# Kernel optimization log

Hardware: AMD Instinct MI355X
Metric: run time of the kernel (lower is better)

The kernel has to match this reference:

```python
import jax, jax.numpy as jnp
import numpy as np

D = 768
H = 12
HD = 64
S = 77
FF = 3072
EPS = 1e-5


def _layernorm(x, w, b):
    mu = jnp.mean(x, axis=-1, keepdims=True)
    var = jnp.mean(jnp.square(x - mu), axis=-1, keepdims=True)
    return (x - mu) * jax.lax.rsqrt(var + EPS) * w + b


def setup_inputs() -> dict:
    key = jax.random.key(0)
    ks = jax.random.split(key, 18)
    s = 1.0 / np.sqrt(D)
    sf = 1.0 / np.sqrt(FF)
    return {
        "x": jax.random.normal(ks[0], (512, S, D), dtype=jnp.float32),
        "ln1_w": jnp.ones((D,), jnp.float32),
        "ln1_b": jnp.zeros((D,), jnp.float32),
        "qw": jax.random.uniform(ks[1], (D, D), jnp.float32, -s, s),
        "qb": jax.random.uniform(ks[2], (D,), jnp.float32, -s, s),
        "kw": jax.random.uniform(ks[3], (D, D), jnp.float32, -s, s),
        "kb": jax.random.uniform(ks[4], (D,), jnp.float32, -s, s),
        "vw": jax.random.uniform(ks[5], (D, D), jnp.float32, -s, s),
        "vb": jax.random.uniform(ks[6], (D,), jnp.float32, -s, s),
        "ow": jax.random.uniform(ks[7], (D, D), jnp.float32, -s, s),
        "ob": jax.random.uniform(ks[8], (D,), jnp.float32, -s, s),
        "ln2_w": jnp.ones((D,), jnp.float32),
        "ln2_b": jnp.zeros((D,), jnp.float32),
        "fc1_w": jax.random.uniform(ks[9], (FF, D), jnp.float32, -s, s),
        "fc1_b": jax.random.uniform(ks[10], (FF,), jnp.float32, -s, s),
        "fc2_w": jax.random.uniform(ks[11], (D, FF), jnp.float32, -sf, sf),
        "fc2_b": jax.random.uniform(ks[12], (D,), jnp.float32, -sf, sf),
    }


def reference(x, ln1_w, ln1_b, qw, qb, kw, kb, vw, vb, ow, ob,
              ln2_w, ln2_b, fc1_w, fc1_b, fc2_w, fc2_b):
    B = x.shape[0]
    # --- attention block ---
    h = _layernorm(x, ln1_w, ln1_b)
    q = (h @ qw.T + qb) * 0.125
    k = h @ kw.T + kb
    v = h @ vw.T + vb
    # [B, S, H, HD] -> [B, H, S, HD]
    q = q.reshape(B, S, H, HD).transpose(0, 2, 1, 3)
    k = k.reshape(B, S, H, HD).transpose(0, 2, 1, 3)
    v = v.reshape(B, S, H, HD).transpose(0, 2, 1, 3)
    scores = jnp.einsum('bhqd,bhkd->bhqk', q, k)  # [B,H,S,S]
    # causal additive mask: -inf strictly above diagonal
    mask = jnp.triu(jnp.full((S, S), -jnp.inf, dtype=scores.dtype), 1)
    scores = scores + mask
    attn = jax.nn.softmax(scores, axis=-1)
    ctx = jnp.einsum('bhqk,bhkd->bhqd', attn, v)  # [B,H,S,HD]
    ctx = ctx.transpose(0, 2, 1, 3).reshape(B, S, D)
    x = x + (ctx @ ow.T + ob)
    # --- MLP block with QuickGELU ---
    res = x
    h2 = _layernorm(x, ln2_w, ln2_b) @ fc1_w.T + fc1_b
    h2 = h2 * jax.nn.sigmoid(h2 * 1.702)
    return res + (h2 @ fc2_w.T + fc2_b)
```

## Files before the change

kernel.cpp:

```cpp
#include <hip/hip_runtime.h>

typedef unsigned short u16;
typedef __bf16 v8bf __attribute__((ext_vector_type(8)));
typedef unsigned short u16x8 __attribute__((ext_vector_type(8)));
typedef float v4f __attribute__((ext_vector_type(4)));

#define DEV __device__ __forceinline__

constexpr int M_TOK = 512 * 77;

DEV u16 f2bf(float f) {
  union { float f; unsigned int u; } v; v.f = f;
  unsigned int r = v.u + 0x7fffu + ((v.u >> 16) & 1u);
  return (u16)(r >> 16);
}

DEV void gload16(const void* g, void* l) {
  __builtin_amdgcn_global_load_lds((const __attribute__((address_space(1))) void*)g,
                                   (__attribute__((address_space(3))) void*)l, 16, 0, 0);
}

DEV v4f MF(v8bf a, v8bf b, v4f c) {
  return __builtin_amdgcn_mfma_f32_16x16x32_bf16(a, b, c, 0, 0, 0);
}

__global__ void cvt4_k(const float* __restrict__ src, u16* __restrict__ dst, int n4, float scale) {
  int i = blockIdx.x * blockDim.x + threadIdx.x;
  if (i >= n4) return;
  const float4 v = ((const float4*)src)[i];
  ushort4 o;
  o.x = f2bf(v.x * scale); o.y = f2bf(v.y * scale);
  o.z = f2bf(v.z * scale); o.w = f2bf(v.w * scale);
  ((ushort4*)dst)[i] = o;
}

__global__ void qkvb_k(const float* __restrict__ qb, const float* __restrict__ kb,
                       const float* __restrict__ vb, float* __restrict__ dst) {
  int i = blockIdx.x * 256 + threadIdx.x;
  if (i >= 2304) return;
  dst[i] = (i < 768) ? qb[i] * 0.125f : (i < 1536 ? kb[i - 768] : vb[i - 1536]);
}

__global__ __launch_bounds__(256) void ln_k(const float* __restrict__ x, const float* __restrict__ w,
                                            const float* __restrict__ bvec, u16* __restrict__ out, int nrows) {
  const int lane = threadIdx.x & 63;
  const int row = blockIdx.x * 4 + (threadIdx.x >> 6);
  if (row >= nrows) return;
  const float4* xr = (const float4*)(x + (size_t)row * 768);
  float4 v[3];
  float sum = 0.f, sq = 0.f;
#pragma unroll
  for (int t = 0; t < 3; ++t) {
    v[t] = xr[lane + 64 * t];
    sum += v[t].x + v[t].y + v[t].z + v[t].w;
    sq  += v[t].x * v[t].x + v[t].y * v[t].y + v[t].z * v[t].z + v[t].w * v[t].w;
  }
#pragma unroll
  for (int o = 1; o < 64; o <<= 1) { sum += __shfl_xor(sum, o, 64); sq += __shfl_xor(sq, o, 64); }
  const float mean = sum * (1.f / 768.f);
  const float inv = rsqrtf(sq * (1.f / 768.f) - mean * mean + 1e-5f);
  u16* orow = out + (size_t)row * 768;
#pragma unroll
  for (int t = 0; t < 3; ++t) {
    const int c = 4 * (lane + 64 * t);
    ushort4 o4;
    o4.x = f2bf((v[t].x - mean) * inv * w[c + 0] + bvec[c + 0]);
    o4.y = f2bf((v[t].y - mean) * inv * w[c + 1] + bvec[c + 1]);
    o4.z = f2bf((v[t].z - mean) * inv * w[c + 2] + bvec[c + 2]);
    o4.w = f2bf((v[t].w - mean) * inv * w[c + 3] + bvec[c + 3]);
    *(ushort4*)(orow + c) = o4;
  }
}

template <int OUTF32, int ACT, int RES>
__global__ __launch_bounds__(512, 4) void gemm_k(
    const u16* __restrict__ A, const u16* __restrict__ Bw,
    const float* __restrict__ bias, const float* __restrict__ res,
    void* __restrict__ out, int M, int N, int K, int nbx) {
  __shared__ u16 lds[24576];
  const int tid = threadIdx.x;
  const int lane = tid & 63;
  const int wv = tid >> 6;
  const int wr = wv >> 2, wc = wv & 3;

  const int nwg = gridDim.x;
  const int q = nwg >> 3, r8 = nwg & 7;
  const int xcd = blockIdx.x & 7, cidx = blockIdx.x >> 3;
  const int wg = (xcd < r8 ? xcd * (q + 1) : r8 * (q + 1) + (xcd - r8) * q) + cidx;
  const int m0 = (wg / nbx) * 128;
  const int n0 = (wg % nbx) * 256;

  const int frow = lane & 15;
  const int fq = lane >> 4;
  const int chunkp = (fq ^ (lane & 3) ^ ((lane >> 2) & 3)) & 3;
  const int aRd = (wr * 64 + frow) * 32 + chunkp * 8;
  const int bRd = 4096 + (wc * 64 + frow) * 32 + chunkp * 8;

  const int srow = tid >> 2;
  const int scg = ((tid & 3) ^ (srow & 3) ^ ((srow >> 2) & 3)) & 3;
  const size_t aBase = (size_t)(m0 + srow) * K + scg * 8;
  const size_t bBase = (size_t)(n0 + srow) * K + scg * 8;
  const int ldsW = wv * 512;

#define GLDA(kt) gload16(A + aBase + (size_t)(kt) * 32, \
                         &lds[(((kt) & 1) ? 12288 : 0) + ldsW])
#define GLDB(kt, g) gload16(Bw + bBase + (size_t)(g) * 128 * K + (size_t)(kt) * 32, \
                            &lds[(((kt) & 1) ? 12288 : 0) + 4096 + ((g) << 12) + ldsW])
#define BAR() asm volatile("s_barrier" ::: "memory")

  v4f acc[4][4];
#pragma unroll
  for (int i = 0; i < 4; ++i)
#pragma unroll
    for (int j = 0; j < 4; ++j) acc[i][j] = (v4f){0.f, 0.f, 0.f, 0.f};

  const int NT = K >> 5;

  GLDA(0); GLDB(0, 0); GLDB(0, 1);
  GLDA(1); GLDB(1, 0); GLDB(1, 1);
  asm volatile("s_waitcnt vmcnt(3)" ::: "memory");
  BAR();

#define KTILE(kt, STG, VM)                                                      \
  do {                                                                          \
    const int sb = ((kt) & 1) ? 12288 : 0;                                      \
    v8bf fa0 = *(const v8bf*)&lds[sb + aRd +    0];                             \
    v8bf fa1 = *(const v8bf*)&lds[sb + aRd +  512];                             \
    v8bf fa2 = *(const v8bf*)&lds[sb + aRd + 1024];                             \
    v8bf fa3 = *(const v8bf*)&lds[sb + aRd + 1536];                             \
    v8bf fb0 = *(const v8bf*)&lds[sb + bRd +    0];                             \
    v8bf fb1 = *(const v8bf*)&lds[sb + bRd +  512];                             \
    v8bf fb2 = *(const v8bf*)&lds[sb + bRd + 1024];                             \
    v8bf fb3 = *(const v8bf*)&lds[sb + bRd + 1536];                             \
    asm volatile("s_waitcnt lgkmcnt(0)" ::: "memory");                          \
    BAR();            \
    if (STG) { GLDA((kt) + 2); GLDB((kt) + 2, 0); GLDB((kt) + 2, 1); }          \
    if ((VM) == 3) asm volatile("s_waitcnt vmcnt(3)" ::: "memory");             \
    else if ((VM) == 0) asm volatile("s_waitcnt vmcnt(0)" ::: "memory");        \
    __builtin_amdgcn_s_setprio(1);                                              \
    acc[0][0] = MF(fa0, fb0, acc[0][0]); acc[0][1] = MF(fa0, fb1, acc[0][1]);   \
    acc[0][2] = MF(fa0, fb2, acc[0][2]); acc[0][3] = MF(fa0, fb3, acc[0][3]);   \
    acc[1][0] = MF(fa1, fb0, acc[1][0]); acc[1][1] = MF(fa1, fb1, acc[1][1]);   \
    acc[1][2] = MF(fa1, fb2, acc[1][2]); acc[1][3] = MF(fa1, fb3, acc[1][3]);   \
    acc[2][0] = MF(fa2, fb0, acc[2][0]); acc[2][1] = MF(fa2, fb1, acc[2][1]);   \
    acc[2][2] = MF(fa2, fb2, acc[2][2]); acc[2][3] = MF(fa2, fb3, acc[2][3]);   \
    acc[3][0] = MF(fa3, fb0, acc[3][0]); acc[3][1] = MF(fa3, fb1, acc[3][1]);   \
    acc[3][2] = MF(fa3, fb2, acc[3][2]); acc[3][3] = MF(fa3, fb3, acc[3][3]);   \
    __builtin_amdgcn_s_setprio(0);                                              \
    BAR();              \
  } while (0)

  for (int kt = 0; kt < NT - 2; ++kt) KTILE(kt, 1, 3);
  KTILE(NT - 2, 0, 0);
  KTILE(NT - 1, 0, -1);
#undef KTILE
#undef GLDA
#undef GLDB
#undef BAR

#pragma unroll
  for (int i = 0; i < 4; ++i) {
    const int rowb = m0 + wr * 64 + i * 16 + fq * 4;
#pragma unroll
    for (int j = 0; j < 4; ++j) {
      const int col = n0 + wc * 64 + j * 16 + frow;
      const float bv = bias[col];
#pragma unroll
      for (int rr = 0; rr < 4; ++rr) {
        float v = acc[i][j][rr] + bv;
        if (ACT) v = v * (1.f / (1.f + __expf(-1.702f * v)));
        const size_t off = (size_t)(rowb + rr) * N + col;
        if (RES) v += res[off];
        if (OUTF32) ((float*)out)[off] = v;
        else ((u16*)out)[off] = f2bf(v);
      }
    }
  }
}

__global__ __launch_bounds__(256) void attn_k(const u16* __restrict__ qkv, u16* __restrict__ ctx) {
  __shared__ u16 sQK[10240];
  __shared__ u16 sVt[64 * 120];
  __shared__ float sS[80][81];
  const int tid = threadIdx.x;
  const int lane = tid & 63;
  const int wv = tid >> 6;
  const int b = blockIdx.x / 12;
  const int h = blockIdx.x % 12;
  u16* sQ = sQK;
  u16* sK = sQK + 5120;
  u16* sP = sQK;

  for (int i = tid; i < 10240 + 64 * 120; i += 256) {
    if (i < 10240) sQK[i] = 0; else sVt[i - 10240] = 0;
  }
  __syncthreads();

  const size_t tokBase = (size_t)(b * 77) * 2304 + h * 64;
  for (int c = tid; c < 77 * 8; c += 256) {
    const int row = c >> 3, k8 = (c & 7) * 8;
    const size_t src = tokBase + (size_t)row * 2304 + k8;
    *(u16x8*)&sQ[row * 64 + k8] = *(const u16x8*)&qkv[src];
    *(u16x8*)&sK[row * 64 + k8] = *(const u16x8*)&qkv[src + 768];
    u16x8 v = *(const u16x8*)&qkv[src + 1536];
#pragma unroll
    for (int j = 0; j < 8; ++j) sVt[(k8 + j) * 120 + row] = v[j];
  }
  __syncthreads();

  const int frow = lane & 15, fk = (lane >> 4) * 8;
  for (int t = wv; t < 25; t += 4) {
    const int it = t / 5, jt = t % 5;
    v4f acc = {0.f, 0.f, 0.f, 0.f};
#pragma unroll
    for (int kk = 0; kk < 2; ++kk) {
      v8bf a = *(const v8bf*)&sQ[(it * 16 + frow) * 64 + kk * 32 + fk];
      v8bf bb = *(const v8bf*)&sK[(jt * 16 + frow) * 64 + kk * 32 + fk];
      acc = MF(a, bb, acc);
    }
    const int col = jt * 16 + frow;
#pragma unroll
    for (int r = 0; r < 4; ++r) {
      const int row = it * 16 + (lane >> 4) * 4 + r;
      sS[row][col] = (col > row) ? -1e30f : acc[r];
    }
  }
  __syncthreads();

  if (tid < 80) {
    const int row = tid;
    float mx = -1e30f;
    for (int c2 = 0; c2 < 80; ++c2) mx = fmaxf(mx, sS[row][c2]);
    float sum = 0.f;
    for (int c2 = 0; c2 < 80; ++c2) { float e = __expf(sS[row][c2] - mx); sum += e; sS[row][c2] = e; }
    const float inv = 1.f / sum;
    for (int c2 = 0; c2 < 80; ++c2) sP[row * 96 + c2] = f2bf(sS[row][c2] * inv);
    for (int c2 = 80; c2 < 96; ++c2) sP[row * 96 + c2] = 0;
  }
  __syncthreads();

  const size_t outBase = (size_t)(b * 77) * 768 + h * 64;
  for (int t = wv; t < 20; t += 4) {
    const int it = t / 4, jt = t % 4;
    v4f acc = {0.f, 0.f, 0.f, 0.f};
#pragma unroll
    for (int kk = 0; kk < 3; ++kk) {
      v8bf a = *(const v8bf*)&sP[(it * 16 + frow) * 96 + kk * 32 + fk];
      v8bf bb = *(const v8bf*)&sVt[(jt * 16 + frow) * 120 + kk * 32 + fk];
      acc = MF(a, bb, acc);
    }
    const int col = jt * 16 + frow;
#pragma unroll
    for (int r = 0; r < 4; ++r) {
      const int row = it * 16 + (lane >> 4) * 4 + r;
      if (row < 77) ctx[outBase + (size_t)row * 768 + col] = f2bf(acc[r]);
    }
  }
}

extern "C" void kernel_launch(void* const* d_in, const int* in_sizes, int n_in,
                              void* d_out, int out_size, void* d_ws, size_t ws_size,
                              hipStream_t stream) {
  const float* x    = (const float*)d_in[0];
  const float* ln1w = (const float*)d_in[1];
  const float* ln1b = (const float*)d_in[2];
  const float* qw   = (const float*)d_in[3];
  const float* qb   = (const float*)d_in[4];
  const float* kw   = (const float*)d_in[5];
  const float* kb   = (const float*)d_in[6];
  const float* vw   = (const float*)d_in[7];
  const float* vb   = (const float*)d_in[8];
  const float* ow   = (const float*)d_in[9];
  const float* ob   = (const float*)d_in[10];
  const float* ln2w = (const float*)d_in[11];
  const float* ln2b = (const float*)d_in[12];
  const float* f1wf = (const float*)d_in[13];
  const float* f1b  = (const float*)d_in[14];
  const float* f2wf = (const float*)d_in[15];
  const float* f2b  = (const float*)d_in[16];
  float* outp = (float*)d_out;

  char* p = (char*)d_ws;
  auto alloc = [&](size_t bytes) { char* r = p; p += (bytes + 255) & ~(size_t)255; return r; };
  u16* wqkv = (u16*)alloc((size_t)2304 * 768 * 2);
  u16* owb  = (u16*)alloc((size_t)768 * 768 * 2);
  u16* f1w  = (u16*)alloc((size_t)3072 * 768 * 2);
  u16* f2w  = (u16*)alloc((size_t)768 * 3072 * 2);
  float* qkvb = (float*)alloc(2304 * 4);
  u16* bufA = (u16*)alloc((size_t)M_TOK * 768 * 2);
  u16* bufB = (u16*)alloc((size_t)M_TOK * 3072 * 2);

  cvt4_k<<<576, 256, 0, stream>>>(qw, wqkv, 147456, 0.125f);
  cvt4_k<<<576, 256, 0, stream>>>(kw, wqkv + 589824, 147456, 1.f);
  cvt4_k<<<576, 256, 0, stream>>>(vw, wqkv + 1179648, 147456, 1.f);
  cvt4_k<<<576, 256, 0, stream>>>(ow, owb, 147456, 1.f);
  cvt4_k<<<2304, 256, 0, stream>>>(f1wf, f1w, 589824, 1.f);
  cvt4_k<<<2304, 256, 0, stream>>>(f2wf, f2w, 589824, 1.f);
  qkvb_k<<<9, 256, 0, stream>>>(qb, kb, vb, qkvb);

  ln_k<<<M_TOK / 4, 256, 0, stream>>>(x, ln1w, ln1b, bufA, M_TOK);
  gemm_k<0, 0, 0><<<308 * 9, 512, 0, stream>>>(bufA, wqkv, qkvb, nullptr, bufB, M_TOK, 2304, 768, 9);
  attn_k<<<512 * 12, 256, 0, stream>>>(bufB, bufA);
  gemm_k<1, 0, 1><<<308 * 3, 512, 0, stream>>>(bufA, owb, ob, x, outp, M_TOK, 768, 768, 3);
  ln_k<<<M_TOK / 4, 256, 0, stream>>>(outp, ln2w, ln2b, bufA, M_TOK);
  gemm_k<0, 1, 0><<<308 * 12, 512, 0, stream>>>(bufA, f1w, f1b, nullptr, bufB, M_TOK, 3072, 768, 12);
  gemm_k<1, 0, 1><<<308 * 3, 512, 0, stream>>>(bufB, f2w, f2b, outp, outp, M_TOK, 768, 3072, 3);
}
```

Baseline: 967.5 us.

## Switch GEMMs to 128x128 tiles with 64-wide K steps and 8-way XOR swizzle

The GEMM kernel's output tile shrinks from 128x256 to 128x128, and the K step grows from 32 to 64 with a new 8-chunk XOR swizzle in LDS. This doubles the number of workgroups per GEMM and halves the number of barrier-separated K iterations. The trade-off is lower arithmetic intensity per tile: each wave now issues 16 MFMAs per iteration from 12 fragment loads, versus 16 from 8 before, so there is more LDS and global traffic per flop. LDS usage rises to 64 KB per block, which may limit occupancy.

```diff
diff --git a/kernel.cpp b/kernel.cpp
--- a/kernel.cpp
+++ b/kernel.cpp
@@ -73,97 +73,99 @@
 }
 
 template <int OUTF32, int ACT, int RES>
-__global__ __launch_bounds__(512, 4) void gemm_k(
+__global__ __launch_bounds__(512, 4) void gemm128_k(
     const u16* __restrict__ A, const u16* __restrict__ Bw,
     const float* __restrict__ bias, const float* __restrict__ res,
     void* __restrict__ out, int M, int N, int K, int nbx) {
-  __shared__ u16 lds[24576];
+  __shared__ u16 lds[32768];
   const int tid = threadIdx.x;
   const int lane = tid & 63;
   const int wv = tid >> 6;
   const int wr = wv >> 2, wc = wv & 3;
 
   const int nwg = gridDim.x;
-  const int q = nwg >> 3, r8 = nwg & 7;
+  const int q8 = nwg >> 3, r8 = nwg & 7;
   const int xcd = blockIdx.x & 7, cidx = blockIdx.x >> 3;
-  const int wg = (xcd < r8 ? xcd * (q + 1) : r8 * (q + 1) + (xcd - r8) * q) + cidx;
+  const int wg = (xcd < r8 ? xcd * (q8 + 1) : r8 * (q8 + 1) + (xcd - r8) * q8) + cidx;
   const int m0 = (wg / nbx) * 128;
-  const int n0 = (wg % nbx) * 256;
-
-  const int frow = lane & 15;
-  const int fq = lane >> 4;
-  const int chunkp = (fq ^ (lane & 3) ^ ((lane >> 2) & 3)) & 3;
-  const int aRd = (wr * 64 + frow) * 32 + chunkp * 8;
-  const int bRd = 4096 + (wc * 64 + frow) * 32 + chunkp * 8;
-
-  const int srow = tid >> 2;
-  const int scg = ((tid & 3) ^ (srow & 3) ^ ((srow >> 2) & 3)) & 3;
-  const size_t aBase = (size_t)(m0 + srow) * K + scg * 8;
-  const size_t bBase = (size_t)(n0 + srow) * K + scg * 8;
+  const int n0 = (wg % nbx) * 128;
+
+  const int frow = lane & 15, fq = lane >> 4;
+  const int e = frow & 7;
+  const int aB0 = (wr * 64 + frow) * 64 + ((fq ^ e) * 8);
+  const int bB0 = 8192 + (wc * 32 + frow) * 64 + ((fq ^ e) * 8);
+
+  const int srow = tid >> 3;
+  const int cOff = ((tid & 7) ^ (srow & 7)) * 8;
+  const u16* pA = A + (size_t)(m0 + srow) * K + cOff;
+  const u16* pB = Bw + (size_t)(n0 + srow) * K + cOff;
+  const size_t hk = (size_t)K * 64;
   const int ldsW = wv * 512;
 
-#define GLDA(kt) gload16(A + aBase + (size_t)(kt) * 32, \
-                         &lds[(((kt) & 1) ? 12288 : 0) + ldsW])
-#define GLDB(kt, g) gload16(Bw + bBase + (size_t)(g) * 128 * K + (size_t)(kt) * 32, \
-                            &lds[(((kt) & 1) ? 12288 : 0) + 4096 + ((g) << 12) + ldsW])
+#define LD(IDX) (*(const v8bf*)&lds[IDX])
 #define BAR() asm volatile("s_barrier" ::: "memory")
-
-  v4f acc[4][4];
+#define VM4() asm volatile("s_waitcnt vmcnt(4)" ::: "memory")
+#define VM0() asm volatile("s_waitcnt vmcnt(0)" ::: "memory")
+#define STA(kt) do { gload16(pA + (size_t)(kt) * 64, &lds[(((kt) & 1) << 14) + ldsW]); \
+                     gload16(pA + hk + (size_t)(kt) * 64, &lds[(((kt) & 1) << 14) + 4096 + ldsW]); } while (0)
+#define STB(kt) do { gload16(pB + (size_t)(kt) * 64, &lds[(((kt) & 1) << 14) + 8192 + ldsW]); \
+                     gload16(pB + hk + (size_t)(kt) * 64, &lds[(((kt) & 1) << 14) + 12288 + ldsW]); } while (0)
+
+  v4f acc[4][2];
 #pragma unroll
   for (int i = 0; i < 4; ++i)
 #pragma unroll
-    for (int j = 0; j < 4; ++j) acc[i][j] = (v4f){0.f, 0.f, 0.f, 0.f};
-
-  const int NT = K >> 5;
-
-  GLDA(0); GLDB(0, 0); GLDB(0, 1);
-  GLDA(1); GLDB(1, 0); GLDB(1, 1);
-  asm volatile("s_waitcnt vmcnt(3)" ::: "memory");
-  BAR();
-
-#define KTILE(kt, STG, VM)                                                      \
+    for (int j = 0; j < 2; ++j) acc[i][j] = (v4f){0.f, 0.f, 0.f, 0.f};
+
+  const int NT = K >> 6;
+
+  STA(0); STB(0);
+  STA(1); STB(1);
+  VM4(); BAR();
+
+#define ITER(kt, STG, VM)                                                       \
   do {                                                                          \
-    const int sb = ((kt) & 1) ? 12288 : 0;                                      \
-    v8bf fa0 = *(const v8bf*)&lds[sb + aRd +    0];                             \
-    v8bf fa1 = *(const v8bf*)&lds[sb + aRd +  512];                             \
-    v8bf fa2 = *(const v8bf*)&lds[sb + aRd + 1024];                             \
-    v8bf fa3 = *(const v8bf*)&lds[sb + aRd + 1536];                             \
-    v8bf fb0 = *(const v8bf*)&lds[sb + bRd +    0];                             \
-    v8bf fb1 = *(const v8bf*)&lds[sb + bRd +  512];                             \
-    v8bf fb2 = *(const v8bf*)&lds[sb + bRd + 1024];                             \
-    v8bf fb3 = *(const v8bf*)&lds[sb + bRd + 1536];                             \
+    const int sb = ((kt) & 1) << 14;                                            \
+    v8bf a0 = LD(sb + aB0), a1 = LD(sb + aB0 + 1024);                           \
+    v8bf a2 = LD(sb + aB0 + 2048), a3 = LD(sb + aB0 + 3072);                    \
+    v8bf b0 = LD(sb + bB0), b1 = LD(sb + bB0 + 1024);                           \
+    v8bf a4 = LD(sb + (aB0 ^ 32)), a5 = LD(sb + (aB0 ^ 32) + 1024);             \
+    v8bf a6 = LD(sb + (aB0 ^ 32) + 2048), a7 = LD(sb + (aB0 ^ 32) + 3072);      \
+    v8bf b2 = LD(sb + (bB0 ^ 32)), b3 = LD(sb + (bB0 ^ 32) + 1024);             \
     asm volatile("s_waitcnt lgkmcnt(0)" ::: "memory");                          \
-    BAR();            \
-    if (STG) { GLDA((kt) + 2); GLDB((kt) + 2, 0); GLDB((kt) + 2, 1); }          \
-    if ((VM) == 3) asm volatile("s_waitcnt vmcnt(3)" ::: "memory");             \
-    else if ((VM) == 0) asm volatile("s_waitcnt vmcnt(0)" ::: "memory");        \
+    BAR();             \
+    if (STG) { STA((kt) + 2); STB((kt) + 2); }                                  \
+    if ((VM) == 4) VM4(); else if ((VM) == 0) VM0();                            \
     __builtin_amdgcn_s_setprio(1);                                              \
-    acc[0][0] = MF(fa0, fb0, acc[0][0]); acc[0][1] = MF(fa0, fb1, acc[0][1]);   \
-    acc[0][2] = MF(fa0, fb2, acc[0][2]); acc[0][3] = MF(fa0, fb3, acc[0][3]);   \
-    acc[1][0] = MF(fa1, fb0, acc[1][0]); acc[1][1] = MF(fa1, fb1, acc[1][1]);   \
-    acc[1][2] = MF(fa1, fb2, acc[1][2]); acc[1][3] = MF(fa1, fb3, acc[1][3]);   \
-    acc[2][0] = MF(fa2, fb0, acc[2][0]); acc[2][1] = MF(fa2, fb1, acc[2][1]);   \
-    acc[2][2] = MF(fa2, fb2, acc[2][2]); acc[2][3] = MF(fa2, fb3, acc[2][3]);   \
-    acc[3][0] = MF(fa3, fb0, acc[3][0]); acc[3][1] = MF(fa3, fb1, acc[3][1]);   \
-    acc[3][2] = MF(fa3, fb2, acc[3][2]); acc[3][3] = MF(fa3, fb3, acc[3][3]);   \
+    acc[0][0] = MF(a0, b0, acc[0][0]); acc[0][1] = MF(a0, b1, acc[0][1]);       \
+    acc[1][0] = MF(a1, b0, acc[1][0]); acc[1][1] = MF(a1, b1, acc[1][1]);       \
+    acc[2][0] = MF(a2, b0, acc[2][0]); acc[2][1] = MF(a2, b1, acc[2][1]);       \
+    acc[3][0] = MF(a3, b0, acc[3][0]); acc[3][1] = MF(a3, b1, acc[3][1]);       \
+    acc[0][0] = MF(a4, b2, acc[0][0]); acc[0][1] = MF(a4, b3, acc[0][1]);       \
+    acc[1][0] = MF(a5, b2, acc[1][0]); acc[1][1] = MF(a5, b3, acc[1][1]);       \
+    acc[2][0] = MF(a6, b2, acc[2][0]); acc[2][1] = MF(a6, b3, acc[2][1]);       \
+    acc[3][0] = MF(a7, b2, acc[3][0]); acc[3][1] = MF(a7, b3, acc[3][1]);       \
     __builtin_amdgcn_s_setprio(0);                                              \
     BAR();              \
   } while (0)
 
-  for (int kt = 0; kt < NT - 2; ++kt) KTILE(kt, 1, 3);
-  KTILE(NT - 2, 0, 0);
-  KTILE(NT - 1, 0, -1);
-#undef KTILE
-#undef GLDA
-#undef GLDB
+  for (int kt = 0; kt < NT - 2; ++kt) ITER(kt, 1, 4);
+  ITER(NT - 2, 0, 0);
+  ITER(NT - 1, 0, -1);
+#undef ITER
+#undef LD
 #undef BAR
+#undef VM4
+#undef VM0
+#undef STA
+#undef STB
 
 #pragma unroll
   for (int i = 0; i < 4; ++i) {
     const int rowb = m0 + wr * 64 + i * 16 + fq * 4;
 #pragma unroll
-    for (int j = 0; j < 4; ++j) {
-      const int col = n0 + wc * 64 + j * 16 + frow;
+    for (int j = 0; j < 2; ++j) {
+      const int col = n0 + wc * 32 + j * 16 + frow;
       const float bv = bias[col];
 #pragma unroll
       for (int rr = 0; rr < 4; ++rr) {
@@ -299,10 +301,10 @@
   qkvb_k<<<9, 256, 0, stream>>>(qb, kb, vb, qkvb);
 
   ln_k<<<M_TOK / 4, 256, 0, stream>>>(x, ln1w, ln1b, bufA, M_TOK);
-  gemm_k<0, 0, 0><<<308 * 9, 512, 0, stream>>>(bufA, wqkv, qkvb, nullptr, bufB, M_TOK, 2304, 768, 9);
+  gemm128_k<0, 0, 0><<<308 * 18, 512, 0, stream>>>(bufA, wqkv, qkvb, nullptr, bufB, M_TOK, 2304, 768, 18);
   attn_k<<<512 * 12, 256, 0, stream>>>(bufB, bufA);
-  gemm_k<1, 0, 1><<<308 * 3, 512, 0, stream>>>(bufA, owb, ob, x, outp, M_TOK, 768, 768, 3);
+  gemm128_k<1, 0, 1><<<308 * 6, 512, 0, stream>>>(bufA, owb, ob, x, outp, M_TOK, 768, 768, 6);
   ln_k<<<M_TOK / 4, 256, 0, stream>>>(outp, ln2w, ln2b, bufA, M_TOK);
-  gemm_k<0, 1, 0><<<308 * 12, 512, 0, stream>>>(bufA, f1w, f1b, nullptr, bufB, M_TOK, 3072, 768, 12);
-  gemm_k<1, 0, 1><<<308 * 3, 512, 0, stream>>>(bufB, f2w, f2b, outp, outp, M_TOK, 768, 3072, 3);
-}
+  gemm128_k<0, 1, 0><<<308 * 24, 512, 0, stream>>>(bufA, f1w, f1b, nullptr, bufB, M_TOK, 3072, 768, 24);
+  gemm128_k<1, 0, 1><<<308 * 6, 512, 0, stream>>>(bufB, f2w, f2b, outp, outp, M_TOK, 768, 3072, 6);
+}
```

Measured after the change: 952.3 us. Within noise of the previous version (-1.6%).
